# Kernel optimization log

Hardware: AMD Instinct MI355X
Metric: run time of the kernel (lower is better)

## Reference

```python
import jax, jax.numpy as jnp
import numpy as np

N = 50000      # nodes
E = 500000     # edges
H = 128        # hidden_channels
P = 1024       # number of (src,dst) link pairs: z==1 and z==2 counts
L = 3          # num_layers
MAXZ = 1000


def setup_inputs() -> dict:
    key = jax.random.key(0)
    ks = jax.random.split(key, 16)
    # z: P src nodes (label 1), P dst nodes (label 2), rest random labels >= 3
    z = jnp.concatenate([
        jnp.ones((P,), jnp.int32),
        jnp.full((P,), 2, jnp.int32),
        jax.random.randint(ks[0], (N - 2 * P,), 3, MAXZ, dtype=jnp.int32),
    ])
    edge_index = jax.random.randint(ks[1], (2, E), 0, N, dtype=jnp.int32)
    batch = jnp.zeros((N,), jnp.int32)  # unused in executed branch
    s = 1.0 / np.sqrt(H)
    z_table = jax.random.normal(ks[2], (MAXZ, H), jnp.float32) * 0.1
    conv_Wl = jax.random.normal(ks[3], (L, H, H), jnp.float32) * s
    conv_bl = jax.random.normal(ks[4], (L, H), jnp.float32) * 0.01
    conv_Wr = jax.random.normal(ks[5], (L, H, H), jnp.float32) * s
    W0 = jax.random.normal(ks[6], (H, H), jnp.float32) * s
    b0 = jax.random.normal(ks[7], (H,), jnp.float32) * 0.01
    W1 = jax.random.normal(ks[8], (H, H), jnp.float32) * s
    b1 = jax.random.normal(ks[9], (H,), jnp.float32) * 0.01
    W2 = jax.random.normal(ks[10], (1, H), jnp.float32) * s
    b2 = jax.random.normal(ks[11], (1,), jnp.float32) * 0.01
    return dict(z=z, edge_index=edge_index, batch=batch, z_table=z_table,
                conv_Wl=conv_Wl, conv_bl=conv_bl, conv_Wr=conv_Wr,
                W0=W0, b0=b0, W1=W1, b1=b1, W2=W2, b2=b2)


def _sage_conv(x, Wl, bl, Wr, src, dst):
    # x: [2, N, H]; mean-aggregate neighbor messages then linear (PyG SAGEConv)
    msgs = x[:, src, :]  # [2, E, H] gather
    agg = jax.vmap(lambda m: jax.ops.segment_sum(m, dst, num_segments=N))(msgs)
    deg = jax.ops.segment_sum(jnp.ones((dst.shape[0],), x.dtype), dst, num_segments=N)
    agg = agg / jnp.maximum(deg, 1.0)[None, :, None]
    return agg @ Wl.T + bl + x @ Wr.T  # lin_l(mean) + bias + lin_r(x)


def reference(z, edge_index, batch, z_table, conv_Wl, conv_bl, conv_Wr,
              W0, b0, W1, b1, W2, b2):
    src, dst = edge_index[0], edge_index[1]
    # ([[1],[2]] == z).long() -> [2, N] in {0,1}; embed -> [2, N, H]
    lbl = (jnp.arange(1, 3, dtype=z.dtype)[:, None] == z[None, :]).astype(jnp.int32)
    x = z_table[lbl]
    for i in range(L - 1):
        x = jax.nn.relu(_sage_conv(x, conv_Wl[i], conv_bl[i], conv_Wr[i], src, dst))
    x = _sage_conv(x, conv_Wl[L - 1], conv_bl[L - 1], conv_Wr[L - 1], src, dst)
    h = jax.nn.relu(x @ W0.T + b0).sum(axis=0)  # [N, H]
    src_idx = jnp.nonzero(z == 1, size=P)[0]
    dst_idx = jnp.nonzero(z == 2, size=P)[0]
    p = h[src_idx] * h[dst_idx]                 # [P, H]
    return jax.nn.relu(p @ W1.T + b1) @ W2.T + b2  # [P, 1]
```

## Files before the change

kernel.cpp:

```cpp
#include <hip/hip_runtime.h>
#include <stdint.h>

#define HH 128
typedef unsigned long long ull;
typedef unsigned short u16;

__device__ __forceinline__ ull shfl_up64(ull v, int d) {
  unsigned lo = (unsigned)__shfl_up((int)(unsigned)(v & 0xffffffffULL), d);
  unsigned hi = (unsigned)__shfl_up((int)(unsigned)(v >> 32), d);
  return ((ull)hi << 32) | (ull)lo;
}
__device__ __forceinline__ ull shfl_down64(ull v, int d) {
  unsigned lo = (unsigned)__shfl_down((int)(unsigned)(v & 0xffffffffULL), d);
  unsigned hi = (unsigned)__shfl_down((int)(unsigned)(v >> 32), d);
  return ((ull)hi << 32) | (ull)lo;
}

__global__ __launch_bounds__(256) void k_ytab(
    const float* __restrict__ zt, const float* __restrict__ Wl0,
    const float* __restrict__ Wr0, const float* __restrict__ Wl2,
    const float* __restrict__ Wr2, const float* __restrict__ bl0,
    const float* __restrict__ bl1, float* __restrict__ y_l,
    float* __restrict__ y_rb, float* __restrict__ vecs_g,
    const int* __restrict__ z, int N, ull* __restrict__ cnt64,
    int* __restrict__ mark) {
  __shared__ float ztS[2][HH];
  __shared__ float vS[4][HH];
  __shared__ float xS[16][HH];
  __shared__ float wAS[32][HH + 1], wBS[32][HH + 1];
  int t = threadIdx.x;
  {
    int gid = blockIdx.x * 256 + t;
    int nthr = gridDim.x * 256;
    for (int n = gid; n < N; n += nthr) {
      cnt64[n] = 0ULL;
      mark[n] = (z[n] <= 2) ? 1 : 0;
    }
  }
  ztS[t >> 7][t & 127] = zt[t];
  __syncthreads();
  int j = t & 127, half = t >> 7;
  int jw = t >> 3, kk0 = (t & 7) * 4;
  float accA = 0.f, accR = 0.f;
  for (int kt = 0; kt < 4; kt++) {
    __syncthreads();
#pragma unroll
    for (int q = 0; q < 4; q++) {
      int jj = q * 32 + jw;
      float4 va = *(const float4*)(Wl0 + (size_t)jj * HH + kt * 32 + kk0);
      float4 vb = *(const float4*)(Wr0 + (size_t)jj * HH + kt * 32 + kk0);
      wAS[kk0 + 0][jj] = va.x; wAS[kk0 + 1][jj] = va.y;
      wAS[kk0 + 2][jj] = va.z; wAS[kk0 + 3][jj] = va.w;
      wBS[kk0 + 0][jj] = vb.x; wBS[kk0 + 1][jj] = vb.y;
      wBS[kk0 + 2][jj] = vb.z; wBS[kk0 + 3][jj] = vb.w;
    }
    __syncthreads();
#pragma unroll
    for (int kk = 0; kk < 32; kk++) {
      float zk = ztS[half][kt * 32 + kk];
      accA = fmaf(zk, wAS[kk][j], accA);
      accR = fmaf(zk, wBS[kk][j], accR);
    }
  }
  __syncthreads();
  vS[half][j] = accA;
  vS[2 + half][j] = accR;
  __syncthreads();
  if (blockIdx.x == 0) {
    vecs_g[t] = vS[t >> 7][t & 127];
    vecs_g[256 + t] = vS[2 + (t >> 7)][t & 127];
  }
  int v0 = blockIdx.x * 16;
#pragma unroll
  for (int rep = 0; rep < 8; rep++) {
    int idx = t + rep * 256;
    int r = idx >> 7, jx = idx & 127;
    int v = v0 + r;
    int d = v >> 4, cnt = (v >> 1) & 7, sel = v & 1;
    float invd = 1.0f / (float)max(d, 1);
    float u1 = (float)cnt * invd, u0 = (float)(d - cnt) * invd;
    xS[r][jx] = fmaxf(fmaf(u0, vS[0][jx], fmaf(u1, vS[1][jx], bl0[jx] + vS[2 + sel][jx])), 0.f);
  }
  int rh = t >> 7;
  float al[8], ar[8];
#pragma unroll
  for (int q = 0; q < 8; q++) { al[q] = 0.f; ar[q] = 0.f; }
  for (int kt = 0; kt < 4; kt++) {
    __syncthreads();
#pragma unroll
    for (int q = 0; q < 4; q++) {
      int jj = q * 32 + jw;
      float4 va = *(const float4*)(Wl2 + (size_t)jj * HH + kt * 32 + kk0);
      float4 vb = *(const float4*)(Wr2 + (size_t)jj * HH + kt * 32 + kk0);
      wAS[kk0 + 0][jj] = va.x; wAS[kk0 + 1][jj] = va.y;
      wAS[kk0 + 2][jj] = va.z; wAS[kk0 + 3][jj] = va.w;
      wBS[kk0 + 0][jj] = vb.x; wBS[kk0 + 1][jj] = vb.y;
      wBS[kk0 + 2][jj] = vb.z; wBS[kk0 + 3][jj] = vb.w;
    }
    __syncthreads();
#pragma unroll
    for (int kk = 0; kk < 32; kk++) {
      float wl = wAS[kk][j], wr = wBS[kk][j];
#pragma unroll
      for (int q = 0; q < 8; q++) {
        float x = xS[rh * 8 + q][kt * 32 + kk];
        al[q] = fmaf(x, wl, al[q]);
        ar[q] = fmaf(x, wr, ar[q]);
      }
    }
  }
  float bb = bl1[j];
#pragma unroll
  for (int q = 0; q < 8; q++) {
    int v = v0 + rh * 8 + q;
    y_l[((size_t)v << 7) + j] = al[q];
    y_rb[((size_t)v << 7) + j] = ar[q] + bb;
  }
}

__global__ void k_edge(const int* __restrict__ z, const int* __restrict__ src,
                       const int* __restrict__ dst, int E,
                       ull* __restrict__ cnt64, int* __restrict__ mark,
                       int* __restrict__ pos) {
  int tid = blockIdx.x * blockDim.x + threadIdx.x;
  int stride = gridDim.x * blockDim.x;
  for (int e = tid; e < E; e += stride) {
    int s = src[e], d = dst[e];
    int zs = z[s];
    ull val = 1ULL | ((ull)(zs == 1) << 20) | ((ull)(zs == 2) << 40);
    ull old = atomicAdd(&cnt64[d], val);
    pos[e] = (int)(old & 0xFFFFF);
    if (z[d] <= 2) mark[s] = 1;
  }
}

__global__ void k_scan1(const ull* __restrict__ cnt64, const int* __restrict__ mark,
                        const int* __restrict__ z, int N,
                        ull* __restrict__ locout, ull* __restrict__ partials) {
  __shared__ ull wsum[4];
  int t = threadIdx.x, b = blockIdx.x;
  int base = b * 1024 + t * 4;
  ull l[4]; ull s = 0;
  for (int i = 0; i < 4; i++) {
    int idx = base + i; ull v = 0;
    if (idx < N) {
      int zz = z[idx];
      v = (cnt64[idx] & 0xFFFFFULL) | ((ull)mark[idx] << 20)
        | ((ull)(zz == 1) << 40) | ((ull)(zz == 2) << 52);
    }
    l[i] = s; s += v;
  }
  int lane = t & 63, wid = t >> 6;
  ull vi = s;
  for (int d2 = 1; d2 < 64; d2 <<= 1) { ull o = shfl_up64(vi, d2); if (lane >= d2) vi += o; }
  if (lane == 63) wsum[wid] = vi;
  __syncthreads();
  ull woff = 0;
  for (int w = 0; w < wid; w++) woff += wsum[w];
  ull thrbase = woff + vi - s;
  for (int i = 0; i < 4; i++) {
    int idx = base + i;
    if (idx < N) locout[idx] = thrbase + l[i];
  }
  if (t == 255) partials[b] = woff + vi;
}

__global__ __launch_bounds__(256) void k_post(const ull* __restrict__ locout, const ull* __restrict__ partials,
                       const int* __restrict__ z, const int* __restrict__ mark,
                       const ull* __restrict__ cnt64,
                       int N, int P, int* __restrict__ rowptr, int* __restrict__ mlist,
                       int* __restrict__ minv, int* __restrict__ plist,
                       int* __restrict__ Rm, int4* __restrict__ pack,
                       u16* __restrict__ keyN) {
  __shared__ ull base_s;
  int t = threadIdx.x;
  if (t < 64) {
    int need = blockIdx.x >> 2;
    ull v = (t < need) ? partials[t] : 0ULL;
    for (int o = 32; o > 0; o >>= 1) v += shfl_down64(v, o);
    if (t == 0) base_s = v;
  }
  __syncthreads();
  int n = blockIdx.x * 256 + t;
  if (n >= N) return;
  ull s = locout[n] + base_s;
  int rp = (int)(s & 0xFFFFF);
  int mp = (int)((s >> 20) & 0xFFFFF);
  int r1 = (int)((s >> 40) & 0xFFF);
  int r2 = (int)(s >> 52);
  rowptr[n] = rp;
  int mk = mark[n];
  if (mk) { mlist[mp] = n; minv[n] = mp; }
  int zz = z[n];
  if (zz == 1) plist[r1] = n;
  else if (zz == 2) plist[P + r2] = n;
  ull cv = cnt64[n];
  int dd = (int)(cv & 0xFFFFF), c1 = (int)((cv >> 20) & 0xFFFFF), c2 = (int)((cv >> 40) & 0xFFFFF);
  pack[n] = make_int4(dd, c1, c2, zz);
  int wcls = (zz == 1) ? 1 : ((zz == 2) ? 2 : 0);
  u16 key;
  if (dd < 64 && c1 < 8 && c2 < 8) key = (u16)(dd | (c1 << 6) | (c2 << 9) | (wcls << 12));
  else key = 0x8000;
  keyN[n] = key;
  if (n == N - 1) *Rm = mp + mk;
}

__global__ void k_csrk(const int* __restrict__ src, const int* __restrict__ dst, int E,
                       const int* __restrict__ rowptr, const int* __restrict__ pos,
                       const u16* __restrict__ keyN, const int* __restrict__ mark,
                       ull* __restrict__ csrk) {
  int e = blockIdx.x * blockDim.x + threadIdx.x;
  if (e >= E) return;
  int d = dst[e];
  if (!mark[d]) return;
  int s = src[e];
  csrk[rowptr[d] + pos[e]] = (ull)(unsigned)s | ((ull)keyN[s] << 32);
}

__device__ __noinline__ float4 yrow_fb(const float* __restrict__ vecs,
    const float* __restrict__ bl0, const float* __restrict__ Wm,
    int j4, int d, int cnt, int sel) {
  float invd = 1.0f / (float)max(d, 1);
  float u1 = (float)cnt * invd, u0 = (float)(d - cnt) * invd;
  const float* Rv = vecs + (2 + sel) * HH;
  float4 acc = make_float4(0, 0, 0, 0);
  for (int k = 0; k < HH; k++) {
    float x = fmaxf(fmaf(u0, vecs[k], fmaf(u1, vecs[HH + k], bl0[k] + Rv[k])), 0.f);
    acc.x = fmaf(x, Wm[(j4 + 0) * HH + k], acc.x);
    acc.y = fmaf(x, Wm[(j4 + 1) * HH + k], acc.y);
    acc.z = fmaf(x, Wm[(j4 + 2) * HH + k], acc.z);
    acc.w = fmaf(x, Wm[(j4 + 3) * HH + k], acc.w);
  }
  return acc;
}

__device__ __forceinline__ float4 yl_fetch(ull cv, int ch, int chsel, int j4,
    const float* __restrict__ y_l, const int4* __restrict__ pack,
    const float* __restrict__ vecs, const float* __restrict__ bl0,
    const float* __restrict__ Wl2) {
  int key = (int)(cv >> 32);
  if (key & 0x8000) {
    int s = (int)(cv & 0xFFFFFFFFULL);
    int4 p = pack[s];
    int cc = ch ? p.z : p.y;
    int sel = (p.w == chsel) ? 1 : 0;
    return yrow_fb(vecs, bl0, Wl2, j4, p.x, cc, sel);
  }
  int cc = (key >> (6 + 3 * ch)) & 7;
  int sel = (((key >> 12) & 3) == chsel) ? 1 : 0;
  int row = ((key & 63) << 4) + (cc << 1) + sel;
  return *(const float4*)(y_l + ((size_t)row << 7) + j4);
}

__global__ __launch_bounds__(256) void k_agg2Y(const int4* __restrict__ pack,
    const ull* __restrict__ csrk, const float* __restrict__ y_l,
    const float* __restrict__ y_rb, const float* __restrict__ vecs,
    const float* __restrict__ bl0, const float* __restrict__ bl1,
    const float* __restrict__ Wl2, const float* __restrict__ Wr2,
    const int* __restrict__ rowptr, const int* __restrict__ mlist,
    const int* __restrict__ Rdev, float* __restrict__ x2c) {
  int gt = blockIdx.x * blockDim.x + threadIdx.x;
  int w = gt >> 6, lane = gt & 63;
  int nw = (gridDim.x * blockDim.x) >> 6;
  int T = *Rdev;
  int ch = lane >> 5, j4 = (lane & 31) * 4;
  int chsel = ch + 1;
  for (int task = w; task < T; task += nw) {
    int n = mlist[task];
    int4 pn = pack[n];
    int beg = rowptr[n], d = pn.x;
    float4 acc = make_float4(0, 0, 0, 0);
    int i = 0;
    for (; i + 4 <= d; i += 4) {
      ull c0 = csrk[beg + i], c1 = csrk[beg + i + 1];
      ull c2 = csrk[beg + i + 2], c3 = csrk[beg + i + 3];
      float4 v0 = yl_fetch(c0, ch, chsel, j4, y_l, pack, vecs, bl0, Wl2);
      float4 v1 = yl_fetch(c1, ch, chsel, j4, y_l, pack, vecs, bl0, Wl2);
      float4 v2 = yl_fetch(c2, ch, chsel, j4, y_l, pack, vecs, bl0, Wl2);
      float4 v3 = yl_fetch(c3, ch, chsel, j4, y_l, pack, vecs, bl0, Wl2);
      acc.x += v0.x + v1.x + v2.x + v3.x;
      acc.y += v0.y + v1.y + v2.y + v3.y;
      acc.z += v0.z + v1.z + v2.z + v3.z;
      acc.w += v0.w + v1.w + v2.w + v3.w;
    }
    for (; i < d; i++) {
      float4 v0 = yl_fetch(csrk[beg + i], ch, chsel, j4, y_l, pack, vecs, bl0, Wl2);
      acc.x += v0.x; acc.y += v0.y; acc.z += v0.z; acc.w += v0.w;
    }
    float inv = 1.0f / (float)max(d, 1);
    int ccn = ch ? pn.z : pn.y;
    int seln = (pn.w == chsel) ? 1 : 0;
    float4 yr;
    if (pn.x < 64 && ccn < 8) {
      yr = *(const float4*)(y_rb + ((size_t)(((pn.x << 3) + ccn) * 2 + seln) << 7) + j4);
    } else {
      yr = yrow_fb(vecs, bl0, Wr2, j4, pn.x, ccn, seln);
      yr.x += bl1[j4]; yr.y += bl1[j4 + 1]; yr.z += bl1[j4 + 2]; yr.w += bl1[j4 + 3];
    }
    float4 o;
    o.x = fmaxf(fmaf(acc.x, inv, yr.x), 0.f);
    o.y = fmaxf(fmaf(acc.y, inv, yr.y), 0.f);
    o.z = fmaxf(fmaf(acc.z, inv, yr.z), 0.f);
    o.w = fmaxf(fmaf(acc.w, inv, yr.w), 0.f);
    *(float4*)(x2c + (size_t)task * 256 + ch * HH + j4) = o;
  }
}

__global__ __launch_bounds__(256) void k_agg3(const float* __restrict__ x2c,
    const ull* __restrict__ csrk, const int* __restrict__ rowptr,
    const int4* __restrict__ pack, const int* __restrict__ plist,
    const int* __restrict__ minv, int T, float* __restrict__ aggp) {
  int gt = blockIdx.x * blockDim.x + threadIdx.x;
  int w = gt >> 6, lane = gt & 63;
  int nw = (gridDim.x * blockDim.x) >> 6;
  int j4 = lane * 4;
  for (int task = w; task < T; task += nw) {
    int n = plist[task];
    int beg = rowptr[n], d = pack[n].x;
    float4 acc = make_float4(0, 0, 0, 0);
    int i = 0;
    for (; i + 4 <= d; i += 4) {
      int m0 = minv[(int)(csrk[beg + i] & 0xFFFFFFFFULL)];
      int m1 = minv[(int)(csrk[beg + i + 1] & 0xFFFFFFFFULL)];
      int m2 = minv[(int)(csrk[beg + i + 2] & 0xFFFFFFFFULL)];
      int m3 = minv[(int)(csrk[beg + i + 3] & 0xFFFFFFFFULL)];
      float4 v0 = *(const float4*)(x2c + (size_t)m0 * 256 + j4);
      float4 v1 = *(const float4*)(x2c + (size_t)m1 * 256 + j4);
      float4 v2 = *(const float4*)(x2c + (size_t)m2 * 256 + j4);
      float4 v3 = *(const float4*)(x2c + (size_t)m3 * 256 + j4);
      acc.x += v0.x + v1.x + v2.x + v3.x;
      acc.y += v0.y + v1.y + v2.y + v3.y;
      acc.z += v0.z + v1.z + v2.z + v3.z;
      acc.w += v0.w + v1.w + v2.w + v3.w;
    }
    for (; i < d; i++) {
      int m0 = minv[(int)(csrk[beg + i] & 0xFFFFFFFFULL)];
      float4 v0 = *(const float4*)(x2c + (size_t)m0 * 256 + j4);
      acc.x += v0.x; acc.y += v0.y; acc.z += v0.z; acc.w += v0.w;
    }
    float inv = 1.0f / (float)max(d, 1);
    float4 o = make_float4(acc.x * inv, acc.y * inv, acc.z * inv, acc.w * inv);
    *(float4*)(aggp + (size_t)task * 256 + j4) = o;
  }
}

#define G3 4
__global__ __launch_bounds__(256) void k_gemm3F(const float* __restrict__ aggp,
    const float* __restrict__ x2c, const float* __restrict__ Wl3,
    const float* __restrict__ Wr3, const float* __restrict__ W0,
    const float* __restrict__ bl2, const float* __restrict__ b0,
    const int* __restrict__ plist, const int* __restrict__ minv,
    float* __restrict__ tmp0) {
  __shared__ float aS[G3][256], xS[G3][256], x3S[G3][256];
  __shared__ float wAS[32][HH + 1], wBS[32][HH + 1];
  int t = threadIdx.x;
  int i0 = blockIdx.x * G3;
  int j = t & 127, c = t >> 7;
#pragma unroll
  for (int g = 0; g < G3; g++) {
    int i = i0 + g;
    aS[g][t] = aggp[(size_t)i * 256 + t];
    xS[g][t] = x2c[(size_t)minv[plist[i]] * 256 + t];
  }
  float acc[G3];
#pragma unroll
  for (int g = 0; g < G3; g++) acc[g] = bl2[j];
  int jw = t >> 3;
  int kk0 = (t & 7) * 4;
  for (int kt = 0; kt < 4; kt++) {
    __syncthreads();
#pragma unroll
    for (int q = 0; q < 4; q++) {
      int jj = q * 32 + jw;
      float4 va = *(const float4*)(Wl3 + (size_t)jj * HH + kt * 32 + kk0);
      float4 vb = *(const float4*)(Wr3 + (size_t)jj * HH + kt * 32 + kk0);
      wAS[kk0 + 0][jj] = va.x; wAS[kk0 + 1][jj] = va.y;
      wAS[kk0 + 2][jj] = va.z; wAS[kk0 + 3][jj] = va.w;
      wBS[kk0 + 0][jj] = vb.x; wBS[kk0 + 1][jj] = vb.y;
      wBS[kk0 + 2][jj] = vb.z; wBS[kk0 + 3][jj] = vb.w;
    }
    __syncthreads();
#pragma unroll
    for (int kk = 0; kk < 32; kk++) {
      int k = kt * 32 + kk;
      float wl = wAS[kk][j], wr = wBS[kk][j];
#pragma unroll
      for (int g = 0; g < G3; g++)
        acc[g] = fmaf(aS[g][c * HH + k], wl, fmaf(xS[g][c * HH + k], wr, acc[g]));
    }
  }
#pragma unroll
  for (int g = 0; g < G3; g++) x3S[g][t] = acc[g];
  float acc2[G3];
#pragma unroll
  for (int g = 0; g < G3; g++) acc2[g] = b0[j];
  for (int kt = 0; kt < 4; kt++) {
    __syncthreads();
#pragma unroll
    for (int q = 0; q < 4; q++) {
      int jj = q * 32 + jw;
      float4 v0 = *(const float4*)(W0 + (size_t)jj * HH + kt * 32 + kk0);
      wAS[kk0 + 0][jj] = v0.x; wAS[kk0 + 1][jj] = v0.y;
      wAS[kk0 + 2][jj] = v0.z; wAS[kk0 + 3][jj] = v0.w;
    }
    __syncthreads();
#pragma unroll
    for (int kk = 0; kk < 32; kk++) {
      int k = kt * 32 + kk;
      float w0v = wAS[kk][j];
#pragma unroll
      for (int g = 0; g < G3; g++)
        acc2[g] = fmaf(x3S[g][c * HH + k], w0v, acc2[g]);
    }
  }
#pragma unroll
  for (int g = 0; g < G3; g++)
    tmp0[(size_t)(2 * (i0 + g) + c) * HH + j] = fmaxf(acc2[g], 0.f);
}

__global__ __launch_bounds__(256) void k_finalP(const float* __restrict__ tmp0,
    const float* __restrict__ W1, const float* __restrict__ b1,
    const float* __restrict__ W2, const float* __restrict__ b2,
    int P, float* __restrict__ out) {
  __shared__ float pS[2][HH];
  __shared__ float wAS[32][HH + 1];
  __shared__ float wred[4];
  int t = threadIdx.x;
  int half = t >> 7, j = t & 127;
  int i = blockIdx.x * 2 + half;
  float hs = tmp0[(size_t)(2 * i) * HH + j] + tmp0[(size_t)(2 * i + 1) * HH + j];
  float hd = tmp0[(size_t)(2 * (i + P)) * HH + j] + tmp0[(size_t)(2 * (i + P) + 1) * HH + j];
  pS[half][j] = hs * hd;
  int jw = t >> 3, kk0 = (t & 7) * 4;
  float acc = b1[j];
  for (int kt = 0; kt < 4; kt++) {
    __syncthreads();
#pragma unroll
    for (int q = 0; q < 4; q++) {
      int jj = q * 32 + jw;
      float4 v = *(const float4*)(W1 + (size_t)jj * HH + kt * 32 + kk0);
      wAS[kk0 + 0][jj] = v.x; wAS[kk0 + 1][jj] = v.y;
      wAS[kk0 + 2][jj] = v.z; wAS[kk0 + 3][jj] = v.w;
    }
    __syncthreads();
#pragma unroll
    for (int kk = 0; kk < 32; kk++)
      acc = fmaf(pS[half][kt * 32 + kk], wAS[kk][j], acc);
  }
  float v = fmaxf(acc, 0.f) * W2[j];
  for (int off = 32; off > 0; off >>= 1) v += __shfl_down(v, off);
  int wid = t >> 6, lane = t & 63;
  if (lane == 0) wred[wid] = v;
  __syncthreads();
  if (t == 0) out[i] = wred[0] + wred[1] + b2[0];
  else if (t == 128) out[i] = wred[2] + wred[3] + b2[0];
}

extern "C" void kernel_launch(void* const* d_in, const int* in_sizes, int n_in,
                              void* d_out, int out_size, void* d_ws, size_t ws_size,
                              hipStream_t stream) {
  const int* z = (const int*)d_in[0];
  const int* ei = (const int*)d_in[1];
  const float* z_table = (const float*)d_in[3];
  const float* conv_Wl = (const float*)d_in[4];
  const float* conv_bl = (const float*)d_in[5];
  const float* conv_Wr = (const float*)d_in[6];
  const float* W0 = (const float*)d_in[7];
  const float* b0 = (const float*)d_in[8];
  const float* W1 = (const float*)d_in[9];
  const float* b1 = (const float*)d_in[10];
  const float* W2 = (const float*)d_in[11];
  const float* b2 = (const float*)d_in[12];
  float* out = (float*)d_out;

  int N = in_sizes[0];
  int E = in_sizes[1] / 2;
  int P = out_size;
  int P2 = 2 * P;
  const int* srcA = ei;
  const int* dstA = ei + E;

  char* basep = (char*)d_ws;
  size_t off = 0;
  auto alloc = [&](size_t bytes) -> char* {
    off = (off + 255) & ~(size_t)255;
    char* pp = basep + off; off += bytes; return pp;
  };
  float* y_l   = (float*)alloc((size_t)1024 * HH * 4);
  float* y_rb  = (float*)alloc((size_t)1024 * HH * 4);
  float* vecs  = (float*)alloc((size_t)4 * HH * 4);
  float* x2c   = (float*)alloc((size_t)N * 256 * 4);
  float* aggp  = (float*)alloc((size_t)P2 * 256 * 4);
  float* tmp0  = (float*)alloc((size_t)2 * P2 * HH * 4);
  ull*   cnt64 = (ull*)alloc((size_t)N * 8);
  int*   mark  = (int*)alloc((size_t)N * 4);
  int*   pos   = (int*)alloc((size_t)E * 4);
  int*   rowptr= (int*)alloc((size_t)N * 4);
  int*   mlist = (int*)alloc((size_t)N * 4);
  int*   minv  = (int*)alloc((size_t)N * 4);
  int*   plist = (int*)alloc((size_t)P2 * 4);
  ull*   csrk  = (ull*)alloc((size_t)E * 8);
  ull*   locout= (ull*)alloc((size_t)N * 8);
  ull*   partials = (ull*)alloc(256 * 8);
  int*   Rm_dev = (int*)alloc(256);
  u16*   keyN  = (u16*)alloc((size_t)N * 2);
  int4*  pack  = (int4*)alloc((size_t)N * 16);
  (void)ws_size; (void)n_in;

  k_ytab<<<64, 256, 0, stream>>>(z_table, conv_Wl, conv_Wr,
                                 conv_Wl + HH * HH, conv_Wr + HH * HH,
                                 conv_bl, conv_bl + HH, y_l, y_rb, vecs,
                                 z, N, cnt64, mark);
  k_edge<<<1024, 256, 0, stream>>>(z, srcA, dstA, E, cnt64, mark, pos);
  int nb = (N + 1023) / 1024;
  k_scan1<<<nb, 256, 0, stream>>>(cnt64, mark, z, N, locout, partials);
  k_post<<<(N + 255) / 256, 256, 0, stream>>>(locout, partials, z, mark, cnt64, N, P,
                                              rowptr, mlist, minv, plist, Rm_dev, pack, keyN);
  k_csrk<<<(E + 255) / 256, 256, 0, stream>>>(srcA, dstA, E, rowptr, pos, keyN, mark, csrk);
  k_agg2Y<<<2048, 256, 0, stream>>>(pack, csrk, y_l, y_rb, vecs, conv_bl, conv_bl + HH,
                                    conv_Wl + HH * HH, conv_Wr + HH * HH,
                                    rowptr, mlist, Rm_dev, x2c);
  k_agg3<<<512, 256, 0, stream>>>(x2c, csrk, rowptr, pack, plist, minv, P2, aggp);
  k_gemm3F<<<P2 / G3, 256, 0, stream>>>(aggp, x2c, conv_Wl + 2 * HH * HH,
                                        conv_Wr + 2 * HH * HH, W0,
                                        conv_bl + 2 * HH, b0, plist, minv, tmp0);
  k_finalP<<<P / 2, 256, 0, stream>>>(tmp0, W1, b1, W2, b2, P, out);
}
```

Measured before the change: 128.1 us.

## Fuse scan with post via decoupled lookback and fuse final MLP into gemm3

Merges the two-pass prefix scan and post-processing kernels into a single kernel that uses an atomic chunk counter and a status/aggregate lookback across blocks. It also folds the final pairwise product and MLP head into the layer-3 GEMM kernel, regrouping tasks so each block holds matching src/dst pairs, which removes the tmp0 round trip. The edge kernel switches from a grid-stride loop to one thread per edge. Together these cut two launches and some intermediate global traffic, at the cost of spin-waiting between blocks in the scan.

```diff
diff --git a/kernel.cpp b/kernel.cpp
--- a/kernel.cpp
+++ b/kernel.cpp
@@ -23,7 +23,7 @@
     const float* __restrict__ bl1, float* __restrict__ y_l,
     float* __restrict__ y_rb, float* __restrict__ vecs_g,
     const int* __restrict__ z, int N, ull* __restrict__ cnt64,
-    int* __restrict__ mark) {
+    int* __restrict__ mark, int* __restrict__ status, int* __restrict__ bctr) {
   __shared__ float ztS[2][HH];
   __shared__ float vS[4][HH];
   __shared__ float xS[16][HH];
@@ -36,6 +36,8 @@
       cnt64[n] = 0ULL;
       mark[n] = (z[n] <= 2) ? 1 : 0;
     }
+    if (gid < 64) status[gid] = 0;
+    if (gid == 0) *bctr = 0;
   }
   ztS[t >> 7][t & 127] = zt[t];
   __syncthreads();
@@ -122,25 +124,33 @@
                        const int* __restrict__ dst, int E,
                        ull* __restrict__ cnt64, int* __restrict__ mark,
                        int* __restrict__ pos) {
-  int tid = blockIdx.x * blockDim.x + threadIdx.x;
-  int stride = gridDim.x * blockDim.x;
-  for (int e = tid; e < E; e += stride) {
-    int s = src[e], d = dst[e];
-    int zs = z[s];
-    ull val = 1ULL | ((ull)(zs == 1) << 20) | ((ull)(zs == 2) << 40);
-    ull old = atomicAdd(&cnt64[d], val);
-    pos[e] = (int)(old & 0xFFFFF);
-    if (z[d] <= 2) mark[s] = 1;
-  }
-}
-
-__global__ void k_scan1(const ull* __restrict__ cnt64, const int* __restrict__ mark,
-                        const int* __restrict__ z, int N,
-                        ull* __restrict__ locout, ull* __restrict__ partials) {
+  int e = blockIdx.x * blockDim.x + threadIdx.x;
+  if (e >= E) return;
+  int s = src[e], d = dst[e];
+  int zs = z[s];
+  ull val = 1ULL | ((ull)(zs == 1) << 20) | ((ull)(zs == 2) << 40);
+  ull old = atomicAdd(&cnt64[d], val);
+  pos[e] = (int)(old & 0xFFFFF);
+  if (z[d] <= 2) mark[s] = 1;
+}
+
+__global__ __launch_bounds__(256) void k_scanpost(
+    const ull* __restrict__ cnt64, const int* __restrict__ mark,
+    const int* __restrict__ z, int N, int P,
+    int* __restrict__ rowptr, int* __restrict__ mlist, int* __restrict__ minv,
+    int* __restrict__ plist, int* __restrict__ Rm, int4* __restrict__ pack,
+    u16* __restrict__ keyN, int* __restrict__ bctr,
+    ull* __restrict__ aggbuf, int* __restrict__ status) {
   __shared__ ull wsum[4];
-  int t = threadIdx.x, b = blockIdx.x;
+  __shared__ int chunk_s;
+  __shared__ ull excl_s;
+  int t = threadIdx.x;
+  if (t == 0) chunk_s = atomicAdd(bctr, 1);
+  __syncthreads();
+  int b = chunk_s;
   int base = b * 1024 + t * 4;
   ull l[4]; ull s = 0;
+#pragma unroll
   for (int i = 0; i < 4; i++) {
     int idx = base + i; ull v = 0;
     if (idx < N) {
@@ -158,51 +168,48 @@
   ull woff = 0;
   for (int w = 0; w < wid; w++) woff += wsum[w];
   ull thrbase = woff + vi - s;
+  if (t == 0) {
+    ull btot = wsum[0] + wsum[1] + wsum[2] + wsum[3];
+    __hip_atomic_store(&aggbuf[b], btot, __ATOMIC_RELAXED, __HIP_MEMORY_SCOPE_AGENT);
+    __hip_atomic_store(&status[b], 1, __ATOMIC_RELEASE, __HIP_MEMORY_SCOPE_AGENT);
+  }
+  if (t < 64) {
+    ull excl = 0;
+    for (int p = lane; p < b; p += 64) {
+      while (__hip_atomic_load(&status[p], __ATOMIC_ACQUIRE, __HIP_MEMORY_SCOPE_AGENT) == 0)
+        __builtin_amdgcn_s_sleep(1);
+      excl += __hip_atomic_load(&aggbuf[p], __ATOMIC_RELAXED, __HIP_MEMORY_SCOPE_AGENT);
+    }
+    for (int o = 32; o > 0; o >>= 1) excl += shfl_down64(excl, o);
+    if (lane == 0) excl_s = excl;
+  }
+  __syncthreads();
+  ull blockbase = excl_s;
+#pragma unroll
   for (int i = 0; i < 4; i++) {
     int idx = base + i;
-    if (idx < N) locout[idx] = thrbase + l[i];
-  }
-  if (t == 255) partials[b] = woff + vi;
-}
-
-__global__ __launch_bounds__(256) void k_post(const ull* __restrict__ locout, const ull* __restrict__ partials,
-                       const int* __restrict__ z, const int* __restrict__ mark,
-                       const ull* __restrict__ cnt64,
-                       int N, int P, int* __restrict__ rowptr, int* __restrict__ mlist,
-                       int* __restrict__ minv, int* __restrict__ plist,
-                       int* __restrict__ Rm, int4* __restrict__ pack,
-                       u16* __restrict__ keyN) {
-  __shared__ ull base_s;
-  int t = threadIdx.x;
-  if (t < 64) {
-    int need = blockIdx.x >> 2;
-    ull v = (t < need) ? partials[t] : 0ULL;
-    for (int o = 32; o > 0; o >>= 1) v += shfl_down64(v, o);
-    if (t == 0) base_s = v;
-  }
-  __syncthreads();
-  int n = blockIdx.x * 256 + t;
-  if (n >= N) return;
-  ull s = locout[n] + base_s;
-  int rp = (int)(s & 0xFFFFF);
-  int mp = (int)((s >> 20) & 0xFFFFF);
-  int r1 = (int)((s >> 40) & 0xFFF);
-  int r2 = (int)(s >> 52);
-  rowptr[n] = rp;
-  int mk = mark[n];
-  if (mk) { mlist[mp] = n; minv[n] = mp; }
-  int zz = z[n];
-  if (zz == 1) plist[r1] = n;
-  else if (zz == 2) plist[P + r2] = n;
-  ull cv = cnt64[n];
-  int dd = (int)(cv & 0xFFFFF), c1 = (int)((cv >> 20) & 0xFFFFF), c2 = (int)((cv >> 40) & 0xFFFFF);
-  pack[n] = make_int4(dd, c1, c2, zz);
-  int wcls = (zz == 1) ? 1 : ((zz == 2) ? 2 : 0);
-  u16 key;
-  if (dd < 64 && c1 < 8 && c2 < 8) key = (u16)(dd | (c1 << 6) | (c2 << 9) | (wcls << 12));
-  else key = 0x8000;
-  keyN[n] = key;
-  if (n == N - 1) *Rm = mp + mk;
+    if (idx >= N) break;
+    ull sf = blockbase + thrbase + l[i];
+    int rp = (int)(sf & 0xFFFFF);
+    int mp = (int)((sf >> 20) & 0xFFFFF);
+    int r1 = (int)((sf >> 40) & 0xFFF);
+    int r2 = (int)(sf >> 52);
+    rowptr[idx] = rp;
+    int mk = mark[idx];
+    if (mk) { mlist[mp] = idx; minv[idx] = mp; }
+    int zz = z[idx];
+    if (zz == 1) plist[r1] = idx;
+    else if (zz == 2) plist[P + r2] = idx;
+    ull cv = cnt64[idx];
+    int dd = (int)(cv & 0xFFFFF), c1 = (int)((cv >> 20) & 0xFFFFF), c2 = (int)((cv >> 40) & 0xFFFFF);
+    pack[idx] = make_int4(dd, c1, c2, zz);
+    int wcls = (zz == 1) ? 1 : ((zz == 2) ? 2 : 0);
+    u16 key;
+    if (dd < 64 && c1 < 8 && c2 < 8) key = (u16)(dd | (c1 << 6) | (c2 << 9) | (wcls << 12));
+    else key = 0x8000;
+    keyN[idx] = key;
+    if (idx == N - 1) *Rm = mp + mk;
+  }
 }
 
 __global__ void k_csrk(const int* __restrict__ src, const int* __restrict__ dst, int E,
@@ -345,20 +352,25 @@
 }
 
 #define G3 4
-__global__ __launch_bounds__(256) void k_gemm3F(const float* __restrict__ aggp,
+__global__ __launch_bounds__(256) void k_gemm3FP(const float* __restrict__ aggp,
     const float* __restrict__ x2c, const float* __restrict__ Wl3,
     const float* __restrict__ Wr3, const float* __restrict__ W0,
-    const float* __restrict__ bl2, const float* __restrict__ b0,
+    const float* __restrict__ W1, const float* __restrict__ bl2,
+    const float* __restrict__ b0, const float* __restrict__ b1,
+    const float* __restrict__ W2, const float* __restrict__ b2,
     const int* __restrict__ plist, const int* __restrict__ minv,
-    float* __restrict__ tmp0) {
+    int P, float* __restrict__ out) {
   __shared__ float aS[G3][256], xS[G3][256], x3S[G3][256];
   __shared__ float wAS[32][HH + 1], wBS[32][HH + 1];
+  __shared__ float pS[2][HH];
+  __shared__ float wred[4];
   int t = threadIdx.x;
-  int i0 = blockIdx.x * G3;
+  int i0 = blockIdx.x * 2;
+  int tsk[G3] = { i0, i0 + 1, P + i0, P + i0 + 1 };
   int j = t & 127, c = t >> 7;
 #pragma unroll
   for (int g = 0; g < G3; g++) {
-    int i = i0 + g;
+    int i = tsk[g];
     aS[g][t] = aggp[(size_t)i * 256 + t];
     xS[g][t] = x2c[(size_t)minv[plist[i]] * 256 + t];
   }
@@ -413,26 +425,17 @@
         acc2[g] = fmaf(x3S[g][c * HH + k], w0v, acc2[g]);
     }
   }
-#pragma unroll
-  for (int g = 0; g < G3; g++)
-    tmp0[(size_t)(2 * (i0 + g) + c) * HH + j] = fmaxf(acc2[g], 0.f);
-}
-
-__global__ __launch_bounds__(256) void k_finalP(const float* __restrict__ tmp0,
-    const float* __restrict__ W1, const float* __restrict__ b1,
-    const float* __restrict__ W2, const float* __restrict__ b2,
-    int P, float* __restrict__ out) {
-  __shared__ float pS[2][HH];
-  __shared__ float wAS[32][HH + 1];
-  __shared__ float wred[4];
-  int t = threadIdx.x;
-  int half = t >> 7, j = t & 127;
-  int i = blockIdx.x * 2 + half;
-  float hs = tmp0[(size_t)(2 * i) * HH + j] + tmp0[(size_t)(2 * i + 1) * HH + j];
-  float hd = tmp0[(size_t)(2 * (i + P)) * HH + j] + tmp0[(size_t)(2 * (i + P) + 1) * HH + j];
-  pS[half][j] = hs * hd;
-  int jw = t >> 3, kk0 = (t & 7) * 4;
-  float acc = b1[j];
+  __syncthreads();
+#pragma unroll
+  for (int g = 0; g < G3; g++) x3S[g][t] = fmaxf(acc2[g], 0.f);
+  __syncthreads();
+  {
+    int p = t >> 7, jx = t & 127;
+    float hs = x3S[p][jx] + x3S[p][HH + jx];
+    float hd = x3S[2 + p][jx] + x3S[2 + p][HH + jx];
+    pS[p][jx] = hs * hd;
+  }
+  float acc3 = b1[j];
   for (int kt = 0; kt < 4; kt++) {
     __syncthreads();
 #pragma unroll
@@ -445,15 +448,15 @@
     __syncthreads();
 #pragma unroll
     for (int kk = 0; kk < 32; kk++)
-      acc = fmaf(pS[half][kt * 32 + kk], wAS[kk][j], acc);
-  }
-  float v = fmaxf(acc, 0.f) * W2[j];
+      acc3 = fmaf(pS[c][kt * 32 + kk], wAS[kk][j], acc3);
+  }
+  float v = fmaxf(acc3, 0.f) * W2[j];
   for (int off = 32; off > 0; off >>= 1) v += __shfl_down(v, off);
   int wid = t >> 6, lane = t & 63;
   if (lane == 0) wred[wid] = v;
   __syncthreads();
-  if (t == 0) out[i] = wred[0] + wred[1] + b2[0];
-  else if (t == 128) out[i] = wred[2] + wred[3] + b2[0];
+  if (t == 0) out[i0] = wred[0] + wred[1] + b2[0];
+  else if (t == 128) out[i0 + 1] = wred[2] + wred[3] + b2[0];
 }
 
 extern "C" void kernel_launch(void* const* d_in, const int* in_sizes, int n_in,
@@ -491,7 +494,6 @@
   float* vecs  = (float*)alloc((size_t)4 * HH * 4);
   float* x2c   = (float*)alloc((size_t)N * 256 * 4);
   float* aggp  = (float*)alloc((size_t)P2 * 256 * 4);
-  float* tmp0  = (float*)alloc((size_t)2 * P2 * HH * 4);
   ull*   cnt64 = (ull*)alloc((size_t)N * 8);
   int*   mark  = (int*)alloc((size_t)N * 4);
   int*   pos   = (int*)alloc((size_t)E * 4);
@@ -500,9 +502,10 @@
   int*   minv  = (int*)alloc((size_t)N * 4);
   int*   plist = (int*)alloc((size_t)P2 * 4);
   ull*   csrk  = (ull*)alloc((size_t)E * 8);
-  ull*   locout= (ull*)alloc((size_t)N * 8);
-  ull*   partials = (ull*)alloc(256 * 8);
-  int*   Rm_dev = (int*)alloc(256);
+  ull*   aggbuf= (ull*)alloc(64 * 8);
+  int*   status= (int*)alloc(64 * 4);
+  int*   bctr  = (int*)alloc(256);
+  int*   Rm_dev= (int*)alloc(256);
   u16*   keyN  = (u16*)alloc((size_t)N * 2);
   int4*  pack  = (int4*)alloc((size_t)N * 16);
   (void)ws_size; (void)n_in;
@@ -510,19 +513,18 @@
   k_ytab<<<64, 256, 0, stream>>>(z_table, conv_Wl, conv_Wr,
                                  conv_Wl + HH * HH, conv_Wr + HH * HH,
                                  conv_bl, conv_bl + HH, y_l, y_rb, vecs,
-                                 z, N, cnt64, mark);
-  k_edge<<<1024, 256, 0, stream>>>(z, srcA, dstA, E, cnt64, mark, pos);
+                                 z, N, cnt64, mark, status, bctr);
+  k_edge<<<(E + 255) / 256, 256, 0, stream>>>(z, srcA, dstA, E, cnt64, mark, pos);
   int nb = (N + 1023) / 1024;
-  k_scan1<<<nb, 256, 0, stream>>>(cnt64, mark, z, N, locout, partials);
-  k_post<<<(N + 255) / 256, 256, 0, stream>>>(locout, partials, z, mark, cnt64, N, P,
-                                              rowptr, mlist, minv, plist, Rm_dev, pack, keyN);
+  k_scanpost<<<nb, 256, 0, stream>>>(cnt64, mark, z, N, P, rowptr, mlist, minv,
+                                     plist, Rm_dev, pack, keyN, bctr, aggbuf, status);
   k_csrk<<<(E + 255) / 256, 256, 0, stream>>>(srcA, dstA, E, rowptr, pos, keyN, mark, csrk);
   k_agg2Y<<<2048, 256, 0, stream>>>(pack, csrk, y_l, y_rb, vecs, conv_bl, conv_bl + HH,
                                     conv_Wl + HH * HH, conv_Wr + HH * HH,
                                     rowptr, mlist, Rm_dev, x2c);
   k_agg3<<<512, 256, 0, stream>>>(x2c, csrk, rowptr, pack, plist, minv, P2, aggp);
-  k_gemm3F<<<P2 / G3, 256, 0, stream>>>(aggp, x2c, conv_Wl + 2 * HH * HH,
-                                        conv_Wr + 2 * HH * HH, W0,
-                                        conv_bl + 2 * HH, b0, plist, minv, tmp0);
-  k_finalP<<<P / 2, 256, 0, stream>>>(tmp0, W1, b1, W2, b2, P, out);
-}
+  k_gemm3FP<<<P / 2, 256, 0, stream>>>(aggp, x2c, conv_Wl + 2 * HH * HH,
+                                       conv_Wr + 2 * HH * HH, W0, W1,
+                                       conv_bl + 2 * HH, b0, b1, W2, b2,
+                                       plist, minv, P, out);
+}
```

After: 130.6 us. No clear change (+1.9%).
